# Kernel optimization log

Measured on AMD Instinct MI355X. Metric: run time of the kernel, lower is better.

## Reference

```python
import jax, jax.numpy as jnp
import numpy as np

MIN_PS = 1       # min_patch_size
MAX_PS = 8       # max_patch_size
LOOKAHEAD = 4
THRESH = 1.2     # entropy_threshold (bits)
PAD = 0          # pad_token


def setup_inputs() -> dict:
    key = jax.random.key(0)
    tokens = jax.random.randint(key, (32, 16384), 0, 8, dtype=jnp.int32)
    return {"tokens": tokens}


def _entropy_per_pos(seq):
    """Shannon entropy (bits) of window seq[p : min(S, p+LOOKAHEAD)] for every p. [S]"""
    S = seq.shape[0]
    idx = jnp.arange(S)[:, None] + jnp.arange(LOOKAHEAD)[None, :]   # [S, L]
    valid = idx < S                                                  # [S, L]
    w = seq[jnp.minimum(idx, S - 1)]                                 # [S, L]
    # count of each element's value within its (masked) window
    eq = (w[:, :, None] == w[:, None, :]) & valid[:, :, None] & valid[:, None, :]
    c = jnp.maximum(eq.sum(-1), 1).astype(jnp.float32)               # [S, L]
    n = valid.sum(-1).astype(jnp.float32)                            # [S]
    # H = -sum_v (c_v/n) log2(c_v/n) = -(1/n) sum_j log2(c_j/n)
    ent = -jnp.where(valid, jnp.log2(c / n[:, None]), 0.0).sum(-1) / n
    return ent


def _patch_one(seq):
    """Vectorized equivalent of AdaptivePatcher._patch_one_sequence.
    Returns padded patches [P,MAX_PS], offsets [P] (-1 pad), num_patches scalar,
    where P = S // MIN_PS (worst case)."""
    S = seq.shape[0]
    hi = _entropy_per_pos(seq) >= THRESH                             # growth stops here
    # next position q >= p with hi[q] (S if none): suffix-min of hi indices
    idx_hi = jnp.where(hi, jnp.arange(S), S)
    next_hi = jax.lax.associative_scan(jnp.minimum, idx_hi, reverse=True)

    max_patches = S // MIN_PS

    def step(i, _):
        valid = i < S
        rem = S - i
        size0 = jnp.minimum(MIN_PS, rem)
        look = jnp.minimum(i + size0, S - 1)
        # grow while size < MAX_PS, i+size < S, ent[i+size] < THRESH
        size = jnp.clip(next_hi[look] - i, size0, jnp.minimum(MAX_PS, rem))
        size = jnp.where(i + size0 >= S, size0, size)   # no room to grow
        size = jnp.where(valid, size, 0)
        off = jnp.where(valid, i, -1)
        return jnp.where(valid, i + size, S), (off, size)

    _, (offsets, sizes) = jax.lax.scan(step, jnp.int32(0), None, length=max_patches)

    pos = offsets[:, None] + jnp.arange(MAX_PS)[None, :]             # [P, MAX_PS]
    mask = jnp.arange(MAX_PS)[None, :] < sizes[:, None]
    patches = jnp.where(mask, seq[jnp.clip(pos, 0, S - 1)], PAD)
    num_patches = (sizes > 0).sum()
    return patches, offsets, num_patches


def reference(tokens):
    # Padded equivalents of the torch module's ragged lists:
    # patches [B, P, MAX_PS], offsets [B, P] (-1 past the end), num_patches [B],
    # cu_seqlens [B+1] (cumulative patch counts).
    patches, offsets, n = jax.vmap(_patch_one)(tokens)
    cu_seqlens = jnp.concatenate(
        [jnp.zeros((1,), jnp.int32), jnp.cumsum(n).astype(jnp.int32)]
    )
    return patches, offsets, n, cu_seqlens
```

## Files before the change

### kernel.cpp

```cpp
#include <hip/hip_runtime.h>


#define S_LEN 16384
#define BATCH 32
#define NCH 8
#define CHUNK 2048
#define NTH 256
#define PPT 8
#define MAX_PS 8
#define MAGIC 0x5A17ULL

__global__ __launch_bounds__(NTH)
void fused_kernel(const int* __restrict__ tokens,
                  int* __restrict__ patches,
                  int* __restrict__ offsets,
                  int* __restrict__ nout,
                  int* __restrict__ cu,
                  unsigned long long* __restrict__ sumPub,
                  unsigned long long* __restrict__ ntotPub)
{
    const int blk = blockIdx.x;
    const int b = blk >> 3, c = blk & 7;
    const int t = threadIdx.x;
    const int lane = t & 63, wv = t >> 6;
    const int cs = c * CHUNK;
    const int p = cs + t * PPT;
    const int* __restrict__ seq = tokens + (size_t)b * S_LEN;
    int* __restrict__ pat = patches + (size_t)b * S_LEN * MAX_PS;
    int* __restrict__ off = offsets + (size_t)b * S_LEN;

    __shared__ unsigned char bs[NTH];
    __shared__ unsigned hw[65];
    __shared__ int partMax[4], partSum[4], red[8];
    __shared__ int anch_s, base_s, ntot_s;

    int v[12];
    int4 a4 = *(const int4*)(seq + p);
    int4 b4 = *(const int4*)(seq + p + 4);
    int4 c4 = make_int4(0, 0, 0, 0);
    if (p + 8 < S_LEN) c4 = *(const int4*)(seq + p + 8);
    v[0]=a4.x; v[1]=a4.y; v[2]=a4.z; v[3]=a4.w;
    v[4]=b4.x; v[5]=b4.y; v[6]=b4.z; v[7]=b4.w;
    v[8]=c4.x; v[9]=c4.y; v[10]=c4.z; v[11]=c4.w;

    unsigned hb = 0;
    int llh = -1, ffh = S_LEN;
#pragma unroll
    for (int k = 0; k < PPT; ++k) {
        int j = p + k;
        int nv = min(4, S_LEN - j);
        unsigned m = 0;
#pragma unroll
        for (int i = 0; i < 4; ++i) if (i < nv) m |= 1u << (v[k + i] & 31);
        int h = (__popc(m) >= 3) ? 1 : 0;
        hb |= (unsigned)h << k;
        if (h) { llh = j; if (ffh == S_LEN) ffh = j; }
    }
    bs[t] = (unsigned char)hb;

    int eh = 0;
    if (t < 7) {
        int j = cs + CHUNK + t;
        if (j < S_LEN) {
            int nv = min(4, S_LEN - j);
            unsigned m = 0;
            for (int i = 0; i < 4; ++i) if (i < nv) m |= 1u << (seq[j + i] & 31);
            eh = (__popc(m) >= 3) ? 1 : 0;
        }
    }
    unsigned long long bal = __ballot(eh);
    if (t == 0) hw[64] = (unsigned)(bal & 0x7f);

    int mx = llh, mn = ffh;
#pragma unroll
    for (int d = 32; d >= 1; d >>= 1) {
        mx = max(mx, __shfl_down(mx, d));
        mn = min(mn, __shfl_down(mn, d));
    }
    if (lane == 0) { red[wv] = mx; red[4 + wv] = mn; }
    int incl = llh;
#pragma unroll
    for (int d = 1; d < 64; d <<= 1) {
        int u = __shfl_up(incl, d);
        if (lane >= d) incl = max(incl, u);
    }
    if (lane == 63) partMax[wv] = incl;
    __syncthreads();

    if (t < 64)
        hw[t] = (unsigned)bs[4*t] | ((unsigned)bs[4*t+1] << 8) |
                ((unsigned)bs[4*t+2] << 16) | ((unsigned)bs[4*t+3] << 24);

    int runx = __shfl_up(incl, 1);
    if (lane == 0) runx = -1;
    for (int w = 0; w < wv; ++w) runx = max(runx, partMax[w]);

    {
        int run = runx, ci = 0;
#pragma unroll
        for (int k = 0; k < PPT; ++k) {
            int j = p + k;
            int h = (hb >> k) & 1;
            int is = h | ((run >= 0) & (((j - run) & 7) == 0));
            ci += is;
            if (h) run = j;
        }
        int s = ci;
#pragma unroll
        for (int d = 32; d >= 1; d >>= 1) s += __shfl_down(s, d);
        if (lane == 0) partSum[wv] = s;
    }
    __syncthreads();

    if (t == 0) {
        int lastHi = max(max(red[0], red[1]), max(red[2], red[3]));
        int fh     = min(min(red[4], red[5]), min(red[6], red[7]));
        int fhl    = min(fh - cs, CHUNK);
        int A      = partSum[0] + partSum[1] + partSum[2] + partSum[3];
        unsigned long long pk = (MAGIC << 48)
                              | ((unsigned long long)(unsigned)(lastHi + 1) << 32)
                              | ((unsigned long long)(unsigned)fhl << 16)
                              | (unsigned long long)(unsigned)A;
        __hip_atomic_store(&sumPub[blk], pk, __ATOMIC_RELAXED, __HIP_MEMORY_SCOPE_AGENT);
    }

    int lh_l = 0, fl_l = 0, A_l = 0;
    if (wv == 0 && lane < c) {
        unsigned long long sv;
        for (;;) {
            sv = __hip_atomic_load(&sumPub[b*NCH + lane], __ATOMIC_RELAXED, __HIP_MEMORY_SCOPE_AGENT);
            if ((sv >> 48) == MAGIC) break;
            __builtin_amdgcn_s_sleep(1);
        }
        lh_l = (int)((sv >> 32) & 0xffff) - 1;
        fl_l = (int)((sv >> 16) & 0xffff);
        A_l  = (int)(sv & 0xffff);
    }
    if (wv == 0) {
        int anchor = -1, base = 0;
        for (int cp = 0; cp < c; ++cp) {
            int lh = __shfl(lh_l, cp);
            int fl = __shfl(fl_l, cp);
            int Ap = __shfl(A_l, cp);
            int lo = cp * CHUNK, hi2 = lo + fl;
            int a = max(anchor, 0);
            base += ((hi2 - a + 7) >> 3) - ((lo - a + 7) >> 3) + Ap;
            if (lh >= 0) anchor = lh;
        }
        if (lane == 0) { anch_s = anchor; base_s = base; }
    }
    __syncthreads();

    int run = max(runx, anch_s);
    unsigned fb = 0;
    int cl = 0;
#pragma unroll
    for (int k = 0; k < PPT; ++k) {
        int j = p + k;
        int h = (hb >> k) & 1;
        int a = max(run, 0);
        int is = h | (((j - a) & 7) == 0);
        fb |= (unsigned)is << k;
        cl += is;
        if (h) run = j;
    }
    int sincl = cl;
#pragma unroll
    for (int d = 1; d < 64; d <<= 1) {
        int u = __shfl_up(sincl, d);
        if (lane >= d) sincl += u;
    }
    if (lane == 63) partSum[wv] = sincl;
    __syncthreads();
    int sexcl = __shfl_up(sincl, 1);
    if (lane == 0) sexcl = 0;
    int r = base_s + sexcl;
    for (int w = 0; w < wv; ++w) r += partSum[w];

    if (c == NCH - 1 && t == 0) {
        int ntot = base_s + partSum[0] + partSum[1] + partSum[2] + partSum[3];
        ntot_s = ntot;
        nout[b] = ntot;
        __hip_atomic_store(&ntotPub[b], (MAGIC << 48) | (unsigned long long)(unsigned)ntot,
                           __ATOMIC_RELAXED, __HIP_MEMORY_SCOPE_AGENT);
    }

#pragma unroll
    for (int k = 0; k < PPT; ++k) {
        if ((fb >> k) & 1u) {
            int j = p + k;
            int lb = t * PPT + k;
            int size = 8;
#pragma unroll
            for (int d = 1; d <= 7; ++d) {
                int bb = lb + d;
                if ((hw[bb >> 5] >> (bb & 31)) & 1u) { size = d; break; }
            }
            size = min(size, S_LEN - j);
            int vals[8];
#pragma unroll
            for (int q = 0; q < 8; ++q) vals[q] = (q < size) ? seq[j + q] : 0;
            off[r] = j;
            int4* dst = (int4*)(pat + (size_t)r * MAX_PS);
            dst[0] = make_int4(vals[0], vals[1], vals[2], vals[3]);
            dst[1] = make_int4(vals[4], vals[5], vals[6], vals[7]);
            ++r;
        }
    }

    __syncthreads();
    if (c == NCH - 1) {
        const int4 z = make_int4(0, 0, 0, 0);
        for (int r2 = ntot_s + t; r2 < S_LEN; r2 += NTH) {
            off[r2] = -1;
            int4* dst = (int4*)(pat + (size_t)r2 * MAX_PS);
            dst[0] = z;
            dst[1] = z;
        }
    }

    if (b == 0 && c == 0 && wv == 0) {
        int nv2 = 0;
        if (lane < BATCH) {
            unsigned long long sv;
            for (;;) {
                sv = __hip_atomic_load(&ntotPub[lane], __ATOMIC_RELAXED, __HIP_MEMORY_SCOPE_AGENT);
                if ((sv >> 48) == MAGIC) break;
                __builtin_amdgcn_s_sleep(1);
            }
            nv2 = (int)(sv & 0xffff);
        }
        int sc2 = nv2;
#pragma unroll
        for (int d = 1; d < 32; d <<= 1) {
            int u = __shfl_up(sc2, d);
            if (lane >= d) sc2 += u;
        }
        if (lane < BATCH) cu[lane + 1] = sc2;
        if (lane == 0) cu[0] = 0;
    }
}

extern "C" void kernel_launch(void* const* d_in, const int* in_sizes, int n_in,
                              void* d_out, int out_size, void* d_ws, size_t ws_size,
                              hipStream_t stream)
{
    const int* tokens = (const int*)d_in[0];
    int* out = (int*)d_out;
    int* patches = out;
    int* offsets = patches + (size_t)BATCH * S_LEN * MAX_PS;
    int* nout    = offsets + (size_t)BATCH * S_LEN;
    int* cu      = nout + BATCH;

    unsigned long long* sumPub  = (unsigned long long*)d_ws;
    unsigned long long* ntotPub = sumPub + BATCH * NCH;

    fused_kernel<<<dim3(BATCH * NCH), dim3(NTH), 0, stream>>>(
        tokens, patches, offsets, nout, cu, sumPub, ntotPub);
}
```

Baseline: 76.57 us.

## Compact patch starts in LDS and emit patches with coalesced thread-per-row writes

Each thread now records its patch start positions into a shared compaction buffer, then the block writes patches so that consecutive threads write consecutive output rows. Token values for patch contents are read from a shared-memory copy of the chunk instead of global memory. This replaces per-thread scattered, divergent writes of up to eight patches with coalesced stores and removes redundant global reads. It costs extra shared memory (about 12 KB) and one more barrier, which may lower occupancy slightly.

```diff
diff --git a/kernel.cpp b/kernel.cpp
--- a/kernel.cpp
+++ b/kernel.cpp
@@ -24,15 +24,18 @@
     const int t = threadIdx.x;
     const int lane = t & 63, wv = t >> 6;
     const int cs = c * CHUNK;
-    const int p = cs + t * PPT;
+    const int pl = t * PPT;
+    const int p = cs + pl;
     const int* __restrict__ seq = tokens + (size_t)b * S_LEN;
     int* __restrict__ pat = patches + (size_t)b * S_LEN * MAX_PS;
     int* __restrict__ off = offsets + (size_t)b * S_LEN;
 
+    __shared__ int tok_s[CHUNK + 8];
+    __shared__ unsigned short rs_s[CHUNK];
     __shared__ unsigned char bs[NTH];
     __shared__ unsigned hw[65];
     __shared__ int partMax[4], partSum[4], red[8];
-    __shared__ int anch_s, base_s, ntot_s;
+    __shared__ int anch_s, base_s, ctot_s, ntot_s;
 
     int v[12];
     int4 a4 = *(const int4*)(seq + p);
@@ -42,6 +45,13 @@
     v[0]=a4.x; v[1]=a4.y; v[2]=a4.z; v[3]=a4.w;
     v[4]=b4.x; v[5]=b4.y; v[6]=b4.z; v[7]=b4.w;
     v[8]=c4.x; v[9]=c4.y; v[10]=c4.z; v[11]=c4.w;
+
+    *(int4*)&tok_s[pl]     = a4;
+    *(int4*)&tok_s[pl + 4] = b4;
+    if (t < 8) {
+        int j2 = cs + CHUNK + t;
+        tok_s[CHUNK + t] = (j2 < S_LEN) ? seq[j2] : 0;
+    }
 
     unsigned hb = 0;
     int llh = -1, ffh = S_LEN;
@@ -174,41 +184,50 @@
     __syncthreads();
     int sexcl = __shfl_up(sincl, 1);
     if (lane == 0) sexcl = 0;
-    int r = base_s + sexcl;
-    for (int w = 0; w < wv; ++w) r += partSum[w];
-
-    if (c == NCH - 1 && t == 0) {
-        int ntot = base_s + partSum[0] + partSum[1] + partSum[2] + partSum[3];
-        ntot_s = ntot;
-        nout[b] = ntot;
-        __hip_atomic_store(&ntotPub[b], (MAGIC << 48) | (unsigned long long)(unsigned)ntot,
-                           __ATOMIC_RELAXED, __HIP_MEMORY_SCOPE_AGENT);
-    }
-
-#pragma unroll
-    for (int k = 0; k < PPT; ++k) {
-        if ((fb >> k) & 1u) {
-            int j = p + k;
-            int lb = t * PPT + k;
-            int size = 8;
-#pragma unroll
-            for (int d = 1; d <= 7; ++d) {
-                int bb = lb + d;
-                if ((hw[bb >> 5] >> (bb & 31)) & 1u) { size = d; break; }
-            }
-            size = min(size, S_LEN - j);
-            int vals[8];
-#pragma unroll
-            for (int q = 0; q < 8; ++q) vals[q] = (q < size) ? seq[j + q] : 0;
-            off[r] = j;
-            int4* dst = (int4*)(pat + (size_t)r * MAX_PS);
-            dst[0] = make_int4(vals[0], vals[1], vals[2], vals[3]);
-            dst[1] = make_int4(vals[4], vals[5], vals[6], vals[7]);
-            ++r;
-        }
-    }
-
-    __syncthreads();
+    int lr = sexcl;
+    for (int w = 0; w < wv; ++w) lr += partSum[w];
+
+    if (t == 0) {
+        int ctot = partSum[0] + partSum[1] + partSum[2] + partSum[3];
+        ctot_s = ctot;
+        if (c == NCH - 1) {
+            int ntot = base_s + ctot;
+            ntot_s = ntot;
+            nout[b] = ntot;
+            __hip_atomic_store(&ntotPub[b], (MAGIC << 48) | (unsigned long long)(unsigned)ntot,
+                               __ATOMIC_RELAXED, __HIP_MEMORY_SCOPE_AGENT);
+        }
+    }
+
+    {
+        int q = lr;
+#pragma unroll
+        for (int k = 0; k < PPT; ++k) {
+            if ((fb >> k) & 1u) rs_s[q++] = (unsigned short)(pl + k);
+        }
+    }
+    __syncthreads();
+
+    const int base = base_s, ctot = ctot_s;
+    for (int r2 = t; r2 < ctot; r2 += NTH) {
+        int pos = rs_s[r2];
+        int j = cs + pos;
+        int size = 8;
+#pragma unroll
+        for (int d = 1; d <= 7; ++d) {
+            int bb = pos + d;
+            if ((hw[bb >> 5] >> (bb & 31)) & 1u) { size = d; break; }
+        }
+        size = min(size, S_LEN - j);
+        int vals[8];
+#pragma unroll
+        for (int q = 0; q < 8; ++q) vals[q] = (q < size) ? tok_s[pos + q] : 0;
+        off[base + r2] = j;
+        int4* dst = (int4*)(pat + (size_t)(base + r2) * MAX_PS);
+        dst[0] = make_int4(vals[0], vals[1], vals[2], vals[3]);
+        dst[1] = make_int4(vals[4], vals[5], vals[6], vals[7]);
+    }
+
     if (c == NCH - 1) {
         const int4 z = make_int4(0, 0, 0, 0);
         for (int r2 = ntot_s + t; r2 < S_LEN; r2 += NTH) {
```

After: 73.63 us. 3.8% less time.
